# Performance work log

Hardware: AMD Instinct MI355X
Metric: run time of the kernel (lower is better)

The kernel has to match this reference:

```python
import jax, jax.numpy as jnp
import numpy as np

B, T, D = 2, 2048, 2048
H, HD = 16, 128
ROPE_BASE = 10000.0
EPS = 1e-6


def setup_inputs() -> dict:
    key = jax.random.key(0)
    ks = jax.random.split(key, 5)
    s = 1.0 / np.sqrt(D)
    return {
        "x": jax.random.normal(ks[0], (B, T, D), dtype=jnp.float32),
        "Wq": jax.random.normal(ks[1], (H * HD, D), dtype=jnp.float32) * s,
        "Wk": jax.random.normal(ks[2], (H * HD, D), dtype=jnp.float32) * s,
        "Wv": jax.random.normal(ks[3], (H * HD, D), dtype=jnp.float32) * s,
        "Wo": jax.random.normal(ks[4], (D, H * HD), dtype=jnp.float32) * s,
        "q_norm_w": jnp.ones((HD,), dtype=jnp.float32),
        "k_norm_w": jnp.ones((HD,), dtype=jnp.float32),
    }


def _rms_norm(x, w):
    # RMSNorm over last dim, no centering (LLaMA/Qwen style)
    norm = jnp.sqrt(jnp.mean(jnp.square(x), axis=-1, keepdims=True) + EPS)
    return x / norm * w


def _rope_interleaved(x):
    # x: (B, T, H, HD); GPT-NeoX interleaved style, sequential positions
    dim = HD // 2
    freqs = jnp.exp(-jnp.arange(0, dim, dtype=jnp.float32) * jnp.log(ROPE_BASE) / dim)
    angles = jnp.arange(T, dtype=jnp.float32)[:, None] * freqs[None, :]  # (T, dim)
    cos = jnp.cos(angles)[None, :, None, :]  # (1, T, 1, dim)
    sin = jnp.sin(angles)[None, :, None, :]
    x_even = x[..., ::2]
    x_odd = x[..., 1::2]
    r_even = x_even * cos - x_odd * sin
    r_odd = x_even * sin + x_odd * cos
    return jnp.stack([r_even, r_odd], axis=-1).reshape(x.shape)


def reference(x, Wq, Wk, Wv, Wo, q_norm_w, k_norm_w):
    # QKV projections (weights stored [out, in], per llm_linear einsum)
    q = jnp.einsum("btd,od->bto", x, Wq).reshape(B, T, H, HD)
    k = jnp.einsum("btd,od->bto", x, Wk).reshape(B, T, H, HD)
    v = jnp.einsum("btd,od->bto", x, Wv).reshape(B, T, H, HD)
    # per-head QK RMSNorm
    q = _rms_norm(q, q_norm_w)
    k = _rms_norm(k, k_norm_w)
    # rotary embeddings
    q = _rope_interleaved(q)
    k = _rope_interleaved(k)
    # causal scaled dot-product attention
    scale = 1.0 / jnp.sqrt(jnp.asarray(HD, dtype=x.dtype))
    scores = jnp.einsum("bthd,bshd->bhts", q, k) * scale  # (B, H, T, T)
    causal = jnp.tril(jnp.ones((T, T), dtype=bool))
    scores = jnp.where(causal[None, None, :, :], scores, jnp.asarray(-1e30, dtype=scores.dtype))
    probs = jax.nn.softmax(scores, axis=-1)
    ctx = jnp.einsum("bhts,bshd->bthd", probs, v).reshape(B, T, H * HD)
    # output projection
    return jnp.einsum("bto,do->btd", ctx, Wo)
```

## Files before the change

kernel.cpp:

```cpp
#include <hip/hip_runtime.h>
#include <cstdint>
#include <cstddef>

#define B_ 2
#define T_ 2048
#define D_ 2048
#define H_ 16
#define HD_ 128
#define EPS_ 1e-6f
#define QSCALE_ 0.08838834764831845f
#define KVSTRIDE_ (H_ * HD_)

typedef unsigned short u16;
typedef short s16x8 __attribute__((ext_vector_type(8)));
typedef float f32x4 __attribute__((ext_vector_type(4)));

__device__ __forceinline__ float bf2f(u16 h) {
  union { unsigned int u; float f; } v;
  v.u = ((unsigned int)h) << 16;
  return v.f;
}
__device__ __forceinline__ u16 f2bf(float f) {
  union { float f; unsigned int u; } v;
  v.f = f;
  unsigned int r = v.u + 0x7FFFu + ((v.u >> 16) & 1u);
  return (u16)(r >> 16);
}

__device__ __forceinline__ void gload16(const void* g, void* l) {
  __builtin_amdgcn_global_load_lds(
      (const __attribute__((address_space(1))) unsigned int*)g,
      (__attribute__((address_space(3))) unsigned int*)l, 16, 0, 0);
}

__global__ void cvt_f32_bf16(const float* __restrict__ in, u16* __restrict__ out, int n4) {
  int i = blockIdx.x * blockDim.x + threadIdx.x;
  if (i < n4) {
    float4 v = ((const float4*)in)[i];
    ((ushort4*)out)[i] = make_ushort4(f2bf(v.x), f2bf(v.y), f2bf(v.z), f2bf(v.w));
  }
}

template <int MODE>
__global__ __launch_bounds__(256, 2) void gemm_btn(const u16* __restrict__ A,
                                                   const u16* __restrict__ Bm,
                                                   void* __restrict__ Cout,
                                                   void* __restrict__ Cout2,
                                                   int M, int N, int K) {
  __shared__ u16 As[2][2 * 128 * 32];
  __shared__ u16 Bs[2][2 * 128 * 32];
  const int tid = threadIdx.x;
  const int w = tid >> 6, lane = tid & 63, quad = lane >> 4, c = lane & 15;
  const int wm = w & 1, wn = w >> 1;
  const int m0 = blockIdx.y * 128, n0 = blockIdx.x * 128;
  const int NT = K >> 6;

  f32x4 acc[4][4];
#pragma unroll
  for (int i = 0; i < 4; ++i)
#pragma unroll
    for (int j = 0; j < 4; ++j) acc[i][j] = (f32x4){0.f, 0.f, 0.f, 0.f};

  auto STAGE = [&](int t, int buf) {
    int k0 = t << 6;
#pragma unroll
    for (int i = 0; i < 4; ++i) {
      int chunk = (w * 4 + i) * 64 + lane;
      int kc = chunk >> 9;
      int within = chunk & 511;
      int row = within >> 2, cc = within & 3;
      gload16(A + (size_t)(m0 + row) * K + k0 + kc * 32 + cc * 8, (void*)(&As[buf][0] + chunk * 8));
      gload16(Bm + (size_t)(n0 + row) * K + k0 + kc * 32 + cc * 8, (void*)(&Bs[buf][0] + chunk * 8));
    }
  };

  STAGE(0, 0);
  STAGE(1, 1);
  asm volatile("s_waitcnt vmcnt(8)" ::: "memory");
  __builtin_amdgcn_s_barrier();

  for (int t = 0; t < NT; ++t) {
    const int cur = t & 1;
    s16x8 af[4][2], bf[4][2];
#pragma unroll
    for (int kc = 0; kc < 2; ++kc) {
#pragma unroll
      for (int mi = 0; mi < 4; ++mi)
        af[mi][kc] = *(const s16x8*)(&As[cur][0] + kc * 4096 + (wm * 64 + mi * 16 + c) * 32 + quad * 8);
#pragma unroll
      for (int ni = 0; ni < 4; ++ni)
        bf[ni][kc] = *(const s16x8*)(&Bs[cur][0] + kc * 4096 + (wn * 64 + ni * 16 + c) * 32 + quad * 8);
    }
    asm volatile("s_waitcnt lgkmcnt(0)" ::: "memory");
    __builtin_amdgcn_s_barrier();
    if (t + 2 < NT) STAGE(t + 2, cur);

#pragma unroll
    for (int kc = 0; kc < 2; ++kc)
#pragma unroll
      for (int mi = 0; mi < 4; ++mi)
#pragma unroll
        for (int ni = 0; ni < 4; ++ni)
          acc[mi][ni] = __builtin_amdgcn_mfma_f32_16x16x32_bf16(af[mi][kc], bf[ni][kc], acc[mi][ni], 0, 0, 0);

    if (t + 1 < NT) {
      if (t + 2 < NT)
        asm volatile("s_waitcnt vmcnt(8)" ::: "memory");
      else
        asm volatile("s_waitcnt vmcnt(0)" ::: "memory");
      __builtin_amdgcn_s_barrier();
    }
  }

  u16* dst16 = (u16*)Cout;
  int coloff = 0, nstride = N;
  if (MODE == 2) {
    nstride = 2048;
    if (n0 >= 2048) { dst16 = (u16*)Cout2; coloff = -2048; }
  }
#pragma unroll
  for (int mi = 0; mi < 4; ++mi)
#pragma unroll
    for (int ni = 0; ni < 4; ++ni)
#pragma unroll
      for (int r = 0; r < 4; ++r) {
        int row = m0 + wm * 64 + mi * 16 + quad * 4 + r;
        int col = n0 + wn * 64 + ni * 16 + c + coloff;
        float v = acc[mi][ni][r];
        if (MODE == 0)
          ((float*)Cout)[(size_t)row * N + col] = v;
        else
          dst16[(size_t)row * nstride + col] = f2bf(v);
      }
}

__global__ void rmsnorm_rope(u16* __restrict__ x, const float* __restrict__ nw, float outscale) {
  const int tid = threadIdx.x;
  const int w = tid >> 6, lane = tid & 63;
  const int vec = blockIdx.x * 4 + w;
  const int t = (vec >> 4) & (T_ - 1);
  u16* base = x + (size_t)vec * HD_;
  unsigned int pk = *(const unsigned int*)(base + lane * 2);
  float e = bf2f((u16)(pk & 0xFFFFu));
  float o = bf2f((u16)(pk >> 16));
  float ss = e * e + o * o;
#pragma unroll
  for (int off = 1; off < 64; off <<= 1) ss += __shfl_xor(ss, off, 64);
  float rn = rsqrtf(ss * (1.0f / HD_) + EPS_);
  float we = nw[lane * 2], wo = nw[lane * 2 + 1];
  e = e * rn * we;
  o = o * rn * wo;
  float freq = expf(-(float)lane * (9.210340371976184f / 64.0f));
  float ang = (float)t * freq;
  float sn, cs;
  sincosf(ang, &sn, &cs);
  float re = (e * cs - o * sn) * outscale;
  float ro = (e * sn + o * cs) * outscale;
  *(unsigned int*)(base + lane * 2) = ((unsigned int)f2bf(ro) << 16) | (unsigned int)f2bf(re);
}

__global__ __launch_bounds__(256, 2) void attn_fwd(const u16* __restrict__ Q,
                                                   const u16* __restrict__ Kg,
                                                   const u16* __restrict__ Vt,
                                                   u16* __restrict__ O) {
  __shared__ u16 Ks[2][64 * 128];
  __shared__ u16 Vts[2][128 * 64];
  __shared__ u16 Ps[64 * 64];
  const int tid = threadIdx.x;
  const int w = tid >> 6, lane = tid & 63, quad = lane >> 4, c = lane & 15;
  const int c7 = (c & 7) * 8;
  const int bid = blockIdx.x;
  const int qt = 31 - (bid >> 5);
  const int h = bid & 15;
  const int b = (bid >> 4) & 1;
  const int q0 = qt * 64;

  s16x8 qf[4];
  const u16* qbase = Q + ((size_t)(b * T_ + q0 + w * 16 + c) * H_ + h) * HD_;
#pragma unroll
  for (int kk = 0; kk < 4; ++kk) qf[kk] = *(const s16x8*)(qbase + kk * 32 + quad * 8);

  f32x4 of[8];
#pragma unroll
  for (int i = 0; i < 8; ++i) of[i] = (f32x4){0.f, 0.f, 0.f, 0.f};
  float m_i[4] = {-1e30f, -1e30f, -1e30f, -1e30f};
  float lp[4] = {0.f, 0.f, 0.f, 0.f};

  const u16* kbase = Kg + ((size_t)b * T_ * H_ + h) * HD_;
  const u16* vtbase = Vt + (size_t)(h * HD_) * (B_ * T_) + (size_t)b * T_;

  auto STAGE = [&](int j, int buf) {
    const u16* krow = kbase + (size_t)(j * 64) * KVSTRIDE_;
    const u16* vrow = vtbase + j * 64;
#pragma unroll
    for (int i = 0; i < 4; ++i) {
      int chunk = i * 256 + tid;
      int krowi = chunk >> 4, kslot = (chunk & 15) ^ (krowi & 7);
      gload16(krow + (size_t)krowi * KVSTRIDE_ + kslot * 8, (void*)(&Ks[buf][0] + chunk * 8));
      int vrowi = chunk >> 3, vslot = (chunk & 7) ^ (vrowi & 7);
      gload16(vrow + (size_t)vrowi * (B_ * T_) + vslot * 8, (void*)(&Vts[buf][0] + chunk * 8));
    }
  };

  STAGE(0, 0);
  __syncthreads();
  int cur = 0;

  for (int j = 0; j <= qt; ++j) {
    if (j < qt) STAGE(j + 1, cur ^ 1);

    f32x4 sf[4];
#pragma unroll
    for (int ni = 0; ni < 4; ++ni) {
      f32x4 a = (f32x4){0.f, 0.f, 0.f, 0.f};
#pragma unroll
      for (int kk = 0; kk < 4; ++kk) {
        s16x8 bfr = *(const s16x8*)(&Ks[cur][(ni * 16 + c) * 128 + ((kk * 32 + quad * 8) ^ c7)]);
        a = __builtin_amdgcn_mfma_f32_16x16x32_bf16(qf[kk], bfr, a, 0, 0, 0);
      }
      sf[ni] = a;
    }
    if (j == qt) {
#pragma unroll
      for (int ni = 0; ni < 4; ++ni)
#pragma unroll
        for (int r = 0; r < 4; ++r) {
          int rowg = w * 16 + quad * 4 + r;
          int colg = ni * 16 + c;
          if (colg > rowg) sf[ni][r] = -1e30f;
        }
    }
    float mc[4];
#pragma unroll
    for (int r = 0; r < 4; ++r)
      mc[r] = fmaxf(fmaxf(sf[0][r], sf[1][r]), fmaxf(sf[2][r], sf[3][r]));
#pragma unroll
    for (int off = 1; off < 16; off <<= 1)
#pragma unroll
      for (int r = 0; r < 4; ++r) mc[r] = fmaxf(mc[r], __shfl_xor(mc[r], off, 64));
#pragma unroll
    for (int r = 0; r < 4; ++r) {
      float mnew = fmaxf(m_i[r], mc[r]);
      float alpha = __expf(m_i[r] - mnew);
      m_i[r] = mnew;
      lp[r] *= alpha;
#pragma unroll
      for (int ot = 0; ot < 8; ++ot) of[ot][r] *= alpha;
    }
#pragma unroll
    for (int ni = 0; ni < 4; ++ni)
#pragma unroll
      for (int r = 0; r < 4; ++r) {
        float p = __expf(sf[ni][r] - m_i[r]);
        sf[ni][r] = p;
        lp[r] += p;
      }
#pragma unroll
    for (int ni = 0; ni < 4; ++ni)
#pragma unroll
      for (int r = 0; r < 4; ++r) {
        int row = w * 16 + quad * 4 + r;
        Ps[row * 64 + ((ni * 16 + c) ^ ((row & 7) * 8))] = f2bf(sf[ni][r]);
      }
    s16x8 pa[2];
    pa[0] = *(const s16x8*)(&Ps[(w * 16 + c) * 64 + ((quad * 8) ^ c7)]);
    pa[1] = *(const s16x8*)(&Ps[(w * 16 + c) * 64 + ((32 + quad * 8) ^ c7)]);
#pragma unroll
    for (int ot = 0; ot < 8; ++ot) {
#pragma unroll
      for (int kk = 0; kk < 2; ++kk) {
        s16x8 vfr = *(const s16x8*)(&Vts[cur][(ot * 16 + c) * 64 + ((kk * 32 + quad * 8) ^ c7)]);
        of[ot] = __builtin_amdgcn_mfma_f32_16x16x32_bf16(pa[kk], vfr, of[ot], 0, 0, 0);
      }
    }

    __syncthreads();
    cur ^= 1;
  }

#pragma unroll
  for (int off = 1; off < 16; off <<= 1)
#pragma unroll
    for (int r = 0; r < 4; ++r) lp[r] += __shfl_xor(lp[r], off, 64);
  float inv[4];
#pragma unroll
  for (int r = 0; r < 4; ++r) inv[r] = 1.0f / lp[r];
  u16* obase = O + ((size_t)(b * T_ + q0) * H_ + h) * HD_;
#pragma unroll
  for (int ot = 0; ot < 8; ++ot)
#pragma unroll
    for (int r = 0; r < 4; ++r)
      obase[(size_t)(w * 16 + quad * 4 + r) * KVSTRIDE_ + ot * 16 + c] = f2bf(of[ot][r] * inv[r]);
}

extern "C" void kernel_launch(void* const* d_in, const int* in_sizes, int n_in,
                              void* d_out, int out_size, void* d_ws, size_t ws_size,
                              hipStream_t stream) {
  const float* x = (const float*)d_in[0];
  const float* Wq = (const float*)d_in[1];
  const float* Wk = (const float*)d_in[2];
  const float* Wv = (const float*)d_in[3];
  const float* Wo = (const float*)d_in[4];
  const float* qw = (const float*)d_in[5];
  const float* kw = (const float*)d_in[6];
  float* out = (float*)d_out;

  const size_t xE = (size_t)B_ * T_ * D_;
  const size_t wE = (size_t)D_ * H_ * HD_;
  const size_t need = xE * 2 * 5 + wE * 2 * 4;
  if (ws_size < need) return;

  char* ws = (char*)d_ws;
  u16* xb = (u16*)ws;    ws += xE * 2;
  u16* wqkb = (u16*)ws;  ws += wE * 2 * 2;
  u16* wvb = (u16*)ws;   ws += wE * 2;
  u16* wob = (u16*)ws;   ws += wE * 2;
  u16* qb = (u16*)ws;    ws += xE * 2;
  u16* kb = (u16*)ws;    ws += xE * 2;
  u16* vtb = (u16*)ws;   ws += xE * 2;
  u16* ctxb = (u16*)ws;  ws += xE * 2;

  cvt_f32_bf16<<<xE / 1024, 256, 0, stream>>>(x, xb, (int)(xE / 4));
  cvt_f32_bf16<<<wE / 1024, 256, 0, stream>>>(Wq, wqkb, (int)(wE / 4));
  cvt_f32_bf16<<<wE / 1024, 256, 0, stream>>>(Wk, wqkb + wE, (int)(wE / 4));
  cvt_f32_bf16<<<wE / 1024, 256, 0, stream>>>(Wv, wvb, (int)(wE / 4));
  cvt_f32_bf16<<<wE / 1024, 256, 0, stream>>>(Wo, wob, (int)(wE / 4));

  dim3 gqk(32, 32);
  gemm_btn<2><<<gqk, 256, 0, stream>>>(xb, wqkb, qb, kb, 4096, 4096, 2048);
  dim3 ggv(32, 16);
  gemm_btn<1><<<ggv, 256, 0, stream>>>(wvb, xb, vtb, nullptr, 2048, 4096, 2048);

  rmsnorm_rope<<<16384, 256, 0, stream>>>(qb, qw, QSCALE_);
  rmsnorm_rope<<<16384, 256, 0, stream>>>(kb, kw, 1.0f);

  attn_fwd<<<B_ * H_ * (T_ / 64), 256, 0, stream>>>(qb, kb, vtb, ctxb);

  dim3 gg(16, 32);
  gemm_btn<0><<<gg, 256, 0, stream>>>(ctxb, wob, out, nullptr, 4096, 2048, 2048);
}
```

Before: 386.9 us.

## Use 128-row query tiles in attention and merge conversion and norm launches

The attention kernel now gives each block 128 query rows, with each wave handling two 16-row MFMA slices. Every staged K/V tile is therefore reused for twice as many queries, and waves skip key tiles that lie entirely above their causal diagonal. The five fp32-to-bf16 conversion launches become one kernel, and the Q and K RMSNorm+RoPE launches become one, to cut launch overhead. The trade-offs are half as many attention blocks, which worsens causal load balance on a large GPU, and more registers per wave.

New measurement: 413.4 us. +6.9%, slower.

```diff
diff --git a/kernel.cpp b/kernel.cpp
--- a/kernel.cpp
+++ b/kernel.cpp
@@ -33,12 +33,22 @@
       (__attribute__((address_space(3))) unsigned int*)l, 16, 0, 0);
 }
 
-__global__ void cvt_f32_bf16(const float* __restrict__ in, u16* __restrict__ out, int n4) {
+__global__ void cvt_all(const float* __restrict__ x, const float* __restrict__ Wq,
+                        const float* __restrict__ Wk, const float* __restrict__ Wv,
+                        const float* __restrict__ Wo, u16* __restrict__ xb,
+                        u16* __restrict__ wqkb, u16* __restrict__ wvb, u16* __restrict__ wob) {
+  const int XQ = 2097152, WQ = 1048576;
   int i = blockIdx.x * blockDim.x + threadIdx.x;
-  if (i < n4) {
-    float4 v = ((const float4*)in)[i];
-    ((ushort4*)out)[i] = make_ushort4(f2bf(v.x), f2bf(v.y), f2bf(v.z), f2bf(v.w));
-  }
+  const float* src;
+  u16* dst;
+  int off;
+  if (i < XQ) { src = x; dst = xb; off = i; }
+  else if (i < XQ + WQ) { src = Wq; dst = wqkb; off = i - XQ; }
+  else if (i < XQ + 2 * WQ) { src = Wk; dst = wqkb + (size_t)WQ * 4; off = i - XQ - WQ; }
+  else if (i < XQ + 3 * WQ) { src = Wv; dst = wvb; off = i - XQ - 2 * WQ; }
+  else { src = Wo; dst = wob; off = i - XQ - 3 * WQ; }
+  float4 v = ((const float4*)src)[off];
+  ((ushort4*)dst)[off] = make_ushort4(f2bf(v.x), f2bf(v.y), f2bf(v.z), f2bf(v.w));
 }
 
 template <int MODE>
@@ -134,10 +144,16 @@
       }
 }
 
-__global__ void rmsnorm_rope(u16* __restrict__ x, const float* __restrict__ nw, float outscale) {
+__global__ void rmsnorm_rope2(u16* __restrict__ qx, u16* __restrict__ kx,
+                              const float* __restrict__ qw, const float* __restrict__ kw) {
   const int tid = threadIdx.x;
   const int w = tid >> 6, lane = tid & 63;
-  const int vec = blockIdx.x * 4 + w;
+  const int bid = blockIdx.x;
+  const bool isq = bid < 16384;
+  u16* x = isq ? qx : kx;
+  const float* nw = isq ? qw : kw;
+  const float outscale = isq ? QSCALE_ : 1.0f;
+  const int vec = (bid & 16383) * 4 + w;
   const int t = (vec >> 4) & (T_ - 1);
   u16* base = x + (size_t)vec * HD_;
   unsigned int pk = *(const unsigned int*)(base + lane * 2);
@@ -165,26 +181,37 @@
                                                    u16* __restrict__ O) {
   __shared__ u16 Ks[2][64 * 128];
   __shared__ u16 Vts[2][128 * 64];
-  __shared__ u16 Ps[64 * 64];
+  __shared__ u16 Ps[128 * 64];
   const int tid = threadIdx.x;
   const int w = tid >> 6, lane = tid & 63, quad = lane >> 4, c = lane & 15;
   const int c7 = (c & 7) * 8;
   const int bid = blockIdx.x;
-  const int qt = 31 - (bid >> 5);
+  const int qtile = 15 - (bid >> 5);
   const int h = bid & 15;
   const int b = (bid >> 4) & 1;
-  const int q0 = qt * 64;
-
-  s16x8 qf[4];
-  const u16* qbase = Q + ((size_t)(b * T_ + q0 + w * 16 + c) * H_ + h) * HD_;
-#pragma unroll
-  for (int kk = 0; kk < 4; ++kk) qf[kk] = *(const s16x8*)(qbase + kk * 32 + quad * 8);
-
-  f32x4 of[8];
-#pragma unroll
-  for (int i = 0; i < 8; ++i) of[i] = (f32x4){0.f, 0.f, 0.f, 0.f};
-  float m_i[4] = {-1e30f, -1e30f, -1e30f, -1e30f};
-  float lp[4] = {0.f, 0.f, 0.f, 0.f};
+  const int q0 = qtile * 128;
+  const int wr0 = q0 + w * 32;
+  const int jmax_blk = 2 * qtile + 1;
+  const int jmax_w = (wr0 + 31) >> 6;
+
+  s16x8 qf[2][4];
+#pragma unroll
+  for (int mi = 0; mi < 2; ++mi) {
+    const u16* qbase = Q + ((size_t)(b * T_ + wr0 + mi * 16 + c) * H_ + h) * HD_;
+#pragma unroll
+    for (int kk = 0; kk < 4; ++kk) qf[mi][kk] = *(const s16x8*)(qbase + kk * 32 + quad * 8);
+  }
+
+  f32x4 of[2][8];
+#pragma unroll
+  for (int mi = 0; mi < 2; ++mi)
+#pragma unroll
+    for (int i = 0; i < 8; ++i) of[mi][i] = (f32x4){0.f, 0.f, 0.f, 0.f};
+  float m_i[2][4], lp[2][4];
+#pragma unroll
+  for (int mi = 0; mi < 2; ++mi)
+#pragma unroll
+    for (int r = 0; r < 4; ++r) { m_i[mi][r] = -1e30f; lp[mi][r] = 0.f; }
 
   const u16* kbase = Kg + ((size_t)b * T_ * H_ + h) * HD_;
   const u16* vtbase = Vt + (size_t)(h * HD_) * (B_ * T_) + (size_t)b * T_;
@@ -206,72 +233,87 @@
   __syncthreads();
   int cur = 0;
 
-  for (int j = 0; j <= qt; ++j) {
-    if (j < qt) STAGE(j + 1, cur ^ 1);
-
-    f32x4 sf[4];
-#pragma unroll
-    for (int ni = 0; ni < 4; ++ni) {
-      f32x4 a = (f32x4){0.f, 0.f, 0.f, 0.f};
-#pragma unroll
-      for (int kk = 0; kk < 4; ++kk) {
-        s16x8 bfr = *(const s16x8*)(&Ks[cur][(ni * 16 + c) * 128 + ((kk * 32 + quad * 8) ^ c7)]);
-        a = __builtin_amdgcn_mfma_f32_16x16x32_bf16(qf[kk], bfr, a, 0, 0, 0);
+  for (int j = 0; j <= jmax_blk; ++j) {
+    if (j < jmax_blk) STAGE(j + 1, cur ^ 1);
+
+    if (j <= jmax_w) {
+      f32x4 sf[2][4];
+#pragma unroll
+      for (int mi = 0; mi < 2; ++mi)
+#pragma unroll
+        for (int ni = 0; ni < 4; ++ni) sf[mi][ni] = (f32x4){0.f, 0.f, 0.f, 0.f};
+#pragma unroll
+      for (int ni = 0; ni < 4; ++ni)
+#pragma unroll
+        for (int kk = 0; kk < 4; ++kk) {
+          s16x8 bfr = *(const s16x8*)(&Ks[cur][(ni * 16 + c) * 128 + ((kk * 32 + quad * 8) ^ c7)]);
+#pragma unroll
+          for (int mi = 0; mi < 2; ++mi)
+            sf[mi][ni] = __builtin_amdgcn_mfma_f32_16x16x32_bf16(qf[mi][kk], bfr, sf[mi][ni], 0, 0, 0);
+        }
+      if (j == jmax_w) {
+#pragma unroll
+        for (int mi = 0; mi < 2; ++mi)
+#pragma unroll
+          for (int ni = 0; ni < 4; ++ni)
+#pragma unroll
+            for (int r = 0; r < 4; ++r) {
+              int rowg = wr0 + mi * 16 + quad * 4 + r;
+              int colg = j * 64 + ni * 16 + c;
+              if (colg > rowg) sf[mi][ni][r] = -1e30f;
+            }
       }
-      sf[ni] = a;
-    }
-    if (j == qt) {
-#pragma unroll
-      for (int ni = 0; ni < 4; ++ni)
+#pragma unroll
+      for (int mi = 0; mi < 2; ++mi) {
+        float mc[4];
+#pragma unroll
+        for (int r = 0; r < 4; ++r)
+          mc[r] = fmaxf(fmaxf(sf[mi][0][r], sf[mi][1][r]), fmaxf(sf[mi][2][r], sf[mi][3][r]));
+#pragma unroll
+        for (int off = 1; off < 16; off <<= 1)
+#pragma unroll
+          for (int r = 0; r < 4; ++r) mc[r] = fmaxf(mc[r], __shfl_xor(mc[r], off, 64));
 #pragma unroll
         for (int r = 0; r < 4; ++r) {
-          int rowg = w * 16 + quad * 4 + r;
-          int colg = ni * 16 + c;
-          if (colg > rowg) sf[ni][r] = -1e30f;
+          float mnew = fmaxf(m_i[mi][r], mc[r]);
+          float alpha = __expf(m_i[mi][r] - mnew);
+          m_i[mi][r] = mnew;
+          lp[mi][r] *= alpha;
+#pragma unroll
+          for (int ot = 0; ot < 8; ++ot) of[mi][ot][r] *= alpha;
         }
-    }
-    float mc[4];
-#pragma unroll
-    for (int r = 0; r < 4; ++r)
-      mc[r] = fmaxf(fmaxf(sf[0][r], sf[1][r]), fmaxf(sf[2][r], sf[3][r]));
-#pragma unroll
-    for (int off = 1; off < 16; off <<= 1)
-#pragma unroll
-      for (int r = 0; r < 4; ++r) mc[r] = fmaxf(mc[r], __shfl_xor(mc[r], off, 64));
-#pragma unroll
-    for (int r = 0; r < 4; ++r) {
-      float mnew = fmaxf(m_i[r], mc[r]);
-      float alpha = __expf(m_i[r] - mnew);
-      m_i[r] = mnew;
-      lp[r] *= alpha;
-#pragma unroll
-      for (int ot = 0; ot < 8; ++ot) of[ot][r] *= alpha;
-    }
-#pragma unroll
-    for (int ni = 0; ni < 4; ++ni)
-#pragma unroll
-      for (int r = 0; r < 4; ++r) {
-        float p = __expf(sf[ni][r] - m_i[r]);
-        sf[ni][r] = p;
-        lp[r] += p;
+#pragma unroll
+        for (int ni = 0; ni < 4; ++ni)
+#pragma unroll
+          for (int r = 0; r < 4; ++r) {
+            float p = __expf(sf[mi][ni][r] - m_i[mi][r]);
+            sf[mi][ni][r] = p;
+            lp[mi][r] += p;
+          }
+#pragma unroll
+        for (int ni = 0; ni < 4; ++ni)
+#pragma unroll
+          for (int r = 0; r < 4; ++r) {
+            int row = w * 32 + mi * 16 + quad * 4 + r;
+            Ps[row * 64 + ((ni * 16 + c) ^ ((row & 7) * 8))] = f2bf(sf[mi][ni][r]);
+          }
       }
-#pragma unroll
-    for (int ni = 0; ni < 4; ++ni)
-#pragma unroll
-      for (int r = 0; r < 4; ++r) {
-        int row = w * 16 + quad * 4 + r;
-        Ps[row * 64 + ((ni * 16 + c) ^ ((row & 7) * 8))] = f2bf(sf[ni][r]);
+      s16x8 pa[2][2];
+#pragma unroll
+      for (int mi = 0; mi < 2; ++mi) {
+        int prow = w * 32 + mi * 16 + c;
+        pa[mi][0] = *(const s16x8*)(&Ps[prow * 64 + ((quad * 8) ^ c7)]);
+        pa[mi][1] = *(const s16x8*)(&Ps[prow * 64 + ((32 + quad * 8) ^ c7)]);
       }
-    s16x8 pa[2];
-    pa[0] = *(const s16x8*)(&Ps[(w * 16 + c) * 64 + ((quad * 8) ^ c7)]);
-    pa[1] = *(const s16x8*)(&Ps[(w * 16 + c) * 64 + ((32 + quad * 8) ^ c7)]);
-#pragma unroll
-    for (int ot = 0; ot < 8; ++ot) {
-#pragma unroll
-      for (int kk = 0; kk < 2; ++kk) {
-        s16x8 vfr = *(const s16x8*)(&Vts[cur][(ot * 16 + c) * 64 + ((kk * 32 + quad * 8) ^ c7)]);
-        of[ot] = __builtin_amdgcn_mfma_f32_16x16x32_bf16(pa[kk], vfr, of[ot], 0, 0, 0);
-      }
+#pragma unroll
+      for (int ot = 0; ot < 8; ++ot)
+#pragma unroll
+        for (int kk = 0; kk < 2; ++kk) {
+          s16x8 vfr = *(const s16x8*)(&Vts[cur][(ot * 16 + c) * 64 + ((kk * 32 + quad * 8) ^ c7)]);
+#pragma unroll
+          for (int mi = 0; mi < 2; ++mi)
+            of[mi][ot] = __builtin_amdgcn_mfma_f32_16x16x32_bf16(pa[mi][kk], vfr, of[mi][ot], 0, 0, 0);
+        }
     }
 
     __syncthreads();
@@ -281,16 +323,21 @@
 #pragma unroll
   for (int off = 1; off < 16; off <<= 1)
 #pragma unroll
-    for (int r = 0; r < 4; ++r) lp[r] += __shfl_xor(lp[r], off, 64);
-  float inv[4];
-#pragma unroll
-  for (int r = 0; r < 4; ++r) inv[r] = 1.0f / lp[r];
-  u16* obase = O + ((size_t)(b * T_ + q0) * H_ + h) * HD_;
-#pragma unroll
-  for (int ot = 0; ot < 8; ++ot)
-#pragma unroll
-    for (int r = 0; r < 4; ++r)
-      obase[(size_t)(w * 16 + quad * 4 + r) * KVSTRIDE_ + ot * 16 + c] = f2bf(of[ot][r] * inv[r]);
+    for (int mi = 0; mi < 2; ++mi)
+#pragma unroll
+      for (int r = 0; r < 4; ++r) lp[mi][r] += __shfl_xor(lp[mi][r], off, 64);
+#pragma unroll
+  for (int mi = 0; mi < 2; ++mi) {
+    float inv[4];
+#pragma unroll
+    for (int r = 0; r < 4; ++r) inv[r] = 1.0f / lp[mi][r];
+    u16* obase = O + ((size_t)(b * T_ + wr0 + mi * 16) * H_ + h) * HD_;
+#pragma unroll
+    for (int ot = 0; ot < 8; ++ot)
+#pragma unroll
+      for (int r = 0; r < 4; ++r)
+        obase[(size_t)(quad * 4 + r) * KVSTRIDE_ + ot * 16 + c] = f2bf(of[mi][ot][r] * inv[r]);
+  }
 }
 
 extern "C" void kernel_launch(void* const* d_in, const int* in_sizes, int n_in,
@@ -320,21 +367,16 @@
   u16* vtb = (u16*)ws;   ws += xE * 2;
   u16* ctxb = (u16*)ws;  ws += xE * 2;
 
-  cvt_f32_bf16<<<xE / 1024, 256, 0, stream>>>(x, xb, (int)(xE / 4));
-  cvt_f32_bf16<<<wE / 1024, 256, 0, stream>>>(Wq, wqkb, (int)(wE / 4));
-  cvt_f32_bf16<<<wE / 1024, 256, 0, stream>>>(Wk, wqkb + wE, (int)(wE / 4));
-  cvt_f32_bf16<<<wE / 1024, 256, 0, stream>>>(Wv, wvb, (int)(wE / 4));
-  cvt_f32_bf16<<<wE / 1024, 256, 0, stream>>>(Wo, wob, (int)(wE / 4));
+  cvt_all<<<24576, 256, 0, stream>>>(x, Wq, Wk, Wv, Wo, xb, wqkb, wvb, wob);
 
   dim3 gqk(32, 32);
   gemm_btn<2><<<gqk, 256, 0, stream>>>(xb, wqkb, qb, kb, 4096, 4096, 2048);
   dim3 ggv(32, 16);
   gemm_btn<1><<<ggv, 256, 0, stream>>>(wvb, xb, vtb, nullptr, 2048, 4096, 2048);
 
-  rmsnorm_rope<<<16384, 256, 0, stream>>>(qb, qw, QSCALE_);
-  rmsnorm_rope<<<16384, 256, 0, stream>>>(kb, kw, 1.0f);
-
-  attn_fwd<<<B_ * H_ * (T_ / 64), 256, 0, stream>>>(qb, kb, vtb, ctxb);
+  rmsnorm_rope2<<<32768, 256, 0, stream>>>(qb, kb, qw, kw);
+
+  attn_fwd<<<B_ * H_ * (T_ / 128), 256, 0, stream>>>(qb, kb, vtb, ctxb);
 
   dim3 gg(16, 32);
   gemm_btn<0><<<gg, 256, 0, stream>>>(ctxb, wob, out, nullptr, 4096, 2048, 2048);
```

## Fuse Q RMSNorm+RoPE into attention, merge casts, raise MFMA priority

Applied to the files above, without the earlier changes.

Q's per-head RMSNorm, RoPE and softmax scaling now run inside the attention kernel's Q-fragment load, with a cross-quad shuffle reduction for the sum of squares. This drops a full read-modify-write pass over Q and one launch. The five fp32-to-bf16 conversion launches become one kernel that picks its source by index range. The attention loop also raises wave priority around its MFMA blocks to favour matrix-core issue. The cost is redundant sincos/exp work per attention block and more register pressure during the prologue.

Result: faster. 374.6 us (-3.2%).

```diff
diff --git a/kernel.cpp b/kernel.cpp
--- a/kernel.cpp
+++ b/kernel.cpp
@@ -33,12 +33,22 @@
       (__attribute__((address_space(3))) unsigned int*)l, 16, 0, 0);
 }
 
-__global__ void cvt_f32_bf16(const float* __restrict__ in, u16* __restrict__ out, int n4) {
+__global__ void cvt_all(const float* __restrict__ x, const float* __restrict__ Wq,
+                        const float* __restrict__ Wk, const float* __restrict__ Wv,
+                        const float* __restrict__ Wo, u16* __restrict__ xb,
+                        u16* __restrict__ wqkb, u16* __restrict__ wvb, u16* __restrict__ wob) {
+  const int XQ = 2097152, WQ = 1048576;
   int i = blockIdx.x * blockDim.x + threadIdx.x;
-  if (i < n4) {
-    float4 v = ((const float4*)in)[i];
-    ((ushort4*)out)[i] = make_ushort4(f2bf(v.x), f2bf(v.y), f2bf(v.z), f2bf(v.w));
-  }
+  const float* src;
+  u16* dst;
+  int off;
+  if (i < XQ) { src = x; dst = xb; off = i; }
+  else if (i < XQ + WQ) { src = Wq; dst = wqkb; off = i - XQ; }
+  else if (i < XQ + 2 * WQ) { src = Wk; dst = wqkb + (size_t)WQ * 4; off = i - XQ - WQ; }
+  else if (i < XQ + 3 * WQ) { src = Wv; dst = wvb; off = i - XQ - 2 * WQ; }
+  else { src = Wo; dst = wob; off = i - XQ - 3 * WQ; }
+  float4 v = ((const float4*)src)[off];
+  ((ushort4*)dst)[off] = make_ushort4(f2bf(v.x), f2bf(v.y), f2bf(v.z), f2bf(v.w));
 }
 
 template <int MODE>
@@ -134,12 +144,12 @@
       }
 }
 
-__global__ void rmsnorm_rope(u16* __restrict__ x, const float* __restrict__ nw, float outscale) {
+__global__ void rmsnorm_rope_k(u16* __restrict__ kx, const float* __restrict__ kw) {
   const int tid = threadIdx.x;
   const int w = tid >> 6, lane = tid & 63;
   const int vec = blockIdx.x * 4 + w;
   const int t = (vec >> 4) & (T_ - 1);
-  u16* base = x + (size_t)vec * HD_;
+  u16* base = kx + (size_t)vec * HD_;
   unsigned int pk = *(const unsigned int*)(base + lane * 2);
   float e = bf2f((u16)(pk & 0xFFFFu));
   float o = bf2f((u16)(pk >> 16));
@@ -147,22 +157,23 @@
 #pragma unroll
   for (int off = 1; off < 64; off <<= 1) ss += __shfl_xor(ss, off, 64);
   float rn = rsqrtf(ss * (1.0f / HD_) + EPS_);
-  float we = nw[lane * 2], wo = nw[lane * 2 + 1];
+  float we = kw[lane * 2], wo = kw[lane * 2 + 1];
   e = e * rn * we;
   o = o * rn * wo;
   float freq = expf(-(float)lane * (9.210340371976184f / 64.0f));
   float ang = (float)t * freq;
   float sn, cs;
   sincosf(ang, &sn, &cs);
-  float re = (e * cs - o * sn) * outscale;
-  float ro = (e * sn + o * cs) * outscale;
+  float re = e * cs - o * sn;
+  float ro = e * sn + o * cs;
   *(unsigned int*)(base + lane * 2) = ((unsigned int)f2bf(ro) << 16) | (unsigned int)f2bf(re);
 }
 
 __global__ __launch_bounds__(256, 2) void attn_fwd(const u16* __restrict__ Q,
                                                    const u16* __restrict__ Kg,
                                                    const u16* __restrict__ Vt,
-                                                   u16* __restrict__ O) {
+                                                   u16* __restrict__ O,
+                                                   const float* __restrict__ qw) {
   __shared__ u16 Ks[2][64 * 128];
   __shared__ u16 Vts[2][128 * 64];
   __shared__ u16 Ps[64 * 64];
@@ -175,10 +186,39 @@
   const int b = (bid >> 4) & 1;
   const int q0 = qt * 64;
 
+  const int trow = q0 + w * 16 + c;
+  const u16* qbase = Q + ((size_t)(b * T_ + trow) * H_ + h) * HD_;
+  s16x8 qraw[4];
+#pragma unroll
+  for (int kk = 0; kk < 4; ++kk) qraw[kk] = *(const s16x8*)(qbase + kk * 32 + quad * 8);
+  float qv[4][8];
+  float ss = 0.f;
+#pragma unroll
+  for (int kk = 0; kk < 4; ++kk)
+#pragma unroll
+    for (int e = 0; e < 8; ++e) {
+      float v = bf2f((u16)qraw[kk][e]);
+      qv[kk][e] = v;
+      ss += v * v;
+    }
+  ss += __shfl_xor(ss, 16, 64);
+  ss += __shfl_xor(ss, 32, 64);
+  float rn = rsqrtf(ss * (1.0f / HD_) + EPS_);
   s16x8 qf[4];
-  const u16* qbase = Q + ((size_t)(b * T_ + q0 + w * 16 + c) * H_ + h) * HD_;
-#pragma unroll
-  for (int kk = 0; kk < 4; ++kk) qf[kk] = *(const s16x8*)(qbase + kk * 32 + quad * 8);
+#pragma unroll
+  for (int kk = 0; kk < 4; ++kk)
+#pragma unroll
+    for (int p = 0; p < 4; ++p) {
+      int idx = kk * 32 + quad * 8 + 2 * p;
+      float e0 = qv[kk][2 * p] * rn * qw[idx];
+      float o0 = qv[kk][2 * p + 1] * rn * qw[idx + 1];
+      float freq = expf(-(float)(idx >> 1) * (9.210340371976184f / 64.0f));
+      float ang = (float)trow * freq;
+      float sn, cs;
+      sincosf(ang, &sn, &cs);
+      qf[kk][2 * p] = (short)f2bf((e0 * cs - o0 * sn) * QSCALE_);
+      qf[kk][2 * p + 1] = (short)f2bf((e0 * sn + o0 * cs) * QSCALE_);
+    }
 
   f32x4 of[8];
 #pragma unroll
@@ -210,6 +250,7 @@
     if (j < qt) STAGE(j + 1, cur ^ 1);
 
     f32x4 sf[4];
+    __builtin_amdgcn_s_setprio(1);
 #pragma unroll
     for (int ni = 0; ni < 4; ++ni) {
       f32x4 a = (f32x4){0.f, 0.f, 0.f, 0.f};
@@ -220,6 +261,7 @@
       }
       sf[ni] = a;
     }
+    __builtin_amdgcn_s_setprio(0);
     if (j == qt) {
 #pragma unroll
       for (int ni = 0; ni < 4; ++ni)
@@ -265,6 +307,7 @@
     s16x8 pa[2];
     pa[0] = *(const s16x8*)(&Ps[(w * 16 + c) * 64 + ((quad * 8) ^ c7)]);
     pa[1] = *(const s16x8*)(&Ps[(w * 16 + c) * 64 + ((32 + quad * 8) ^ c7)]);
+    __builtin_amdgcn_s_setprio(1);
 #pragma unroll
     for (int ot = 0; ot < 8; ++ot) {
 #pragma unroll
@@ -273,6 +316,7 @@
         of[ot] = __builtin_amdgcn_mfma_f32_16x16x32_bf16(pa[kk], vfr, of[ot], 0, 0, 0);
       }
     }
+    __builtin_amdgcn_s_setprio(0);
 
     __syncthreads();
     cur ^= 1;
@@ -320,21 +364,16 @@
   u16* vtb = (u16*)ws;   ws += xE * 2;
   u16* ctxb = (u16*)ws;  ws += xE * 2;
 
-  cvt_f32_bf16<<<xE / 1024, 256, 0, stream>>>(x, xb, (int)(xE / 4));
-  cvt_f32_bf16<<<wE / 1024, 256, 0, stream>>>(Wq, wqkb, (int)(wE / 4));
-  cvt_f32_bf16<<<wE / 1024, 256, 0, stream>>>(Wk, wqkb + wE, (int)(wE / 4));
-  cvt_f32_bf16<<<wE / 1024, 256, 0, stream>>>(Wv, wvb, (int)(wE / 4));
-  cvt_f32_bf16<<<wE / 1024, 256, 0, stream>>>(Wo, wob, (int)(wE / 4));
+  cvt_all<<<24576, 256, 0, stream>>>(x, Wq, Wk, Wv, Wo, xb, wqkb, wvb, wob);
 
   dim3 gqk(32, 32);
   gemm_btn<2><<<gqk, 256, 0, stream>>>(xb, wqkb, qb, kb, 4096, 4096, 2048);
   dim3 ggv(32, 16);
   gemm_btn<1><<<ggv, 256, 0, stream>>>(wvb, xb, vtb, nullptr, 2048, 4096, 2048);
 
-  rmsnorm_rope<<<16384, 256, 0, stream>>>(qb, qw, QSCALE_);
-  rmsnorm_rope<<<16384, 256, 0, stream>>>(kb, kw, 1.0f);
-
-  attn_fwd<<<B_ * H_ * (T_ / 64), 256, 0, stream>>>(qb, kb, vtb, ctxb);
+  rmsnorm_rope_k<<<16384, 256, 0, stream>>>(kb, kw);
+
+  attn_fwd<<<B_ * H_ * (T_ / 64), 256, 0, stream>>>(qb, kb, vtb, ctxb, qw);
 
   dim3 gg(16, 32);
   gemm_btn<0><<<gg, 256, 0, stream>>>(ctxb, wob, out, nullptr, 4096, 2048, 2048);
```
